# Performance work log

Hardware: AMD Instinct MI355X
Metric: run time of the kernel (lower is better)

The kernel has to match this reference:

```python
import jax, jax.numpy as jnp
import numpy as np

N_NODES = 100000
DEG = 16          # regular-graph degree so degrees[start] > 0 for all nodes
STEPS = 32
D_FEAT = 16
MAXI32 = 2147483647


def setup_inputs() -> dict:
    key = jax.random.key(0)
    k1, k2, k3 = jax.random.split(key, 3)
    x = jax.random.normal(k1, (N_NODES, D_FEAT), dtype=jnp.float32)
    # CSR-style flat adjacency list: node v's neighbors are
    # adj_nodes[adj_offset[v] : adj_offset[v] + degrees[v]]
    adj_nodes = jax.random.randint(k2, (N_NODES * DEG,), 0, N_NODES, dtype=jnp.int32)
    adj_offset = (jnp.arange(N_NODES, dtype=jnp.int32) * DEG)
    degrees = jnp.full((N_NODES,), DEG, dtype=jnp.int32)
    # cache of random integers, one per (step, walk), as in the torch code
    choices = jax.random.randint(k3, (STEPS, N_NODES), 0, MAXI32, dtype=jnp.int32)
    return {"x": x, "adj_nodes": adj_nodes, "adj_offset": adj_offset,
            "degrees": degrees, "choices": choices}


def reference(x, adj_nodes, adj_offset, degrees, choices):
    """Non-backtracking random walk (Walker.sample_walks with start_p=1.0,
    all nodes having degree > 0, so start = arange(n)).
    Returns walks [steps+1, w] and walk_edges [steps, w]."""
    n = degrees.shape[0]
    nb_degrees = jnp.maximum(degrees - 1, 1)  # reduced degree for non-backtrack rewrite
    start = jnp.arange(n, dtype=jnp.int32)

    def step(carry, ch):
        prev, cur = carry                      # [w] previous / current nodes
        deg = degrees[cur]
        edge_idx = ch % deg                    # unweighted modulo edge choice
        chosen = adj_offset[cur] + edge_idx
        new = adj_nodes[chosen]
        bt = new == prev                       # backtracking walks
        # conditional rewrite: pick a different outgoing edge
        alt = adj_offset[cur] + (edge_idx + 1 + ch % nb_degrees[cur]) % deg
        chosen = jnp.where(bt, alt, chosen)
        new = jnp.where(bt, adj_nodes[alt], new)
        return (cur, new), (new, chosen)

    # prev = -1 at step 0 => bt is all-False, matching the i > 0 guard
    prev0 = jnp.full_like(start, -1)
    _, (nodes, walk_edges) = jax.lax.scan(step, (prev0, start), choices)
    walks = jnp.concatenate([start[None, :], nodes], axis=0)  # [steps+1, w]
    return walks, walk_edges
```

## Files before the change

### kernel.cpp

```cpp
#include <hip/hip_runtime.h>
#include <hip/hip_bf16.h>


#define DEG 16

__global__ void check_kernel(const int* __restrict__ degrees,
                             const int* __restrict__ adj_offset,
                             int n, int* __restrict__ flag) {
    int v = blockIdx.x * blockDim.x + threadIdx.x;
    if (v < n) {
        if (degrees[v] != DEG || adj_offset[v] != v * DEG)
            atomicOr(flag, 1);
    }
}

template <int STEPS>
__global__ __launch_bounds__(256) void walker_fast(
    const int* __restrict__ adj_nodes,
    const int* __restrict__ adj_offset,
    const int* __restrict__ degrees,
    const int* __restrict__ choices,
    int* __restrict__ out, int n,
    const int* __restrict__ flag) {

    int w = blockIdx.x * blockDim.x + threadIdx.x;
    if (w >= n) return;

    int* walks      = out;
    int* walk_edges = out + (STEPS + 1) * n;
    walks[w] = w;

    if (*flag == 0) {
        int chs[STEPS];
#pragma unroll
        for (int i = 0; i < STEPS; ++i) chs[i] = choices[i * n + w];

        int prev = -1, cur = w;
#pragma unroll
        for (int i = 0; i < STEPS; ++i) {
            int ch   = chs[i];
            int e    = ch & (DEG - 1);
            int base = cur << 4;
            int chosen = base + e;
            int alt    = base + ((e + 1 + ch % (DEG - 1)) & (DEG - 1));

            int nw0 = adj_nodes[chosen];
            int nw1 = adj_nodes[alt];

            bool bt = (nw0 == prev);
            int nw  = bt ? nw1 : nw0;
            walks[(i + 1) * n + w] = nw;
            walk_edges[i * n + w]  = bt ? alt : chosen;
            prev = cur;
            cur  = nw;
        }
    } else {
        int prev = -1, cur = w;
        for (int i = 0; i < STEPS; ++i) {
            int ch  = choices[i * n + w];
            int deg = degrees[cur];
            int off = adj_offset[cur];
            int nb  = deg - 1 > 1 ? deg - 1 : 1;

            int e      = ch % deg;
            int chosen = off + e;
            int alt    = off + (e + 1 + ch % nb) % deg;

            int nw0 = adj_nodes[chosen];
            int nw1 = adj_nodes[alt];

            bool bt = (nw0 == prev);
            int nw  = bt ? nw1 : nw0;
            walks[(i + 1) * n + w] = nw;
            walk_edges[i * n + w]  = bt ? alt : chosen;
            prev = cur;
            cur  = nw;
        }
    }
}

__global__ __launch_bounds__(256) void walker_generic(
    const int* __restrict__ adj_nodes,
    const int* __restrict__ adj_offset,
    const int* __restrict__ degrees,
    const int* __restrict__ choices,
    int* __restrict__ out, int n, int steps) {

    int w = blockIdx.x * blockDim.x + threadIdx.x;
    if (w >= n) return;

    int* walks      = out;
    int* walk_edges = out + (steps + 1) * n;
    walks[w] = w;

    int prev = -1, cur = w;
    for (int i = 0; i < steps; ++i) {
        int ch  = choices[i * n + w];
        int deg = degrees[cur];
        int off = adj_offset[cur];
        int nb  = deg - 1 > 1 ? deg - 1 : 1;

        int e      = ch % deg;
        int chosen = off + e;
        int alt    = off + (e + 1 + ch % nb) % deg;

        int nw0 = adj_nodes[chosen];
        int nw1 = adj_nodes[alt];

        bool bt = (nw0 == prev);
        int nw  = bt ? nw1 : nw0;
        walks[(i + 1) * n + w] = nw;
        walk_edges[i * n + w]  = bt ? alt : chosen;
        prev = cur;
        cur  = nw;
    }
}

extern "C" void kernel_launch(void* const* d_in, const int* in_sizes, int n_in,
                              void* d_out, int out_size, void* d_ws, size_t ws_size,
                              hipStream_t stream) {
    const int* adj_nodes  = (const int*)d_in[1];
    const int* adj_offset = (const int*)d_in[2];
    const int* degrees    = (const int*)d_in[3];
    const int* choices    = (const int*)d_in[4];
    int* out  = (int*)d_out;
    int* flag = (int*)d_ws;

    int n     = in_sizes[2];
    int steps = in_sizes[4] / n;

    int block = 256;
    int grid  = (n + block - 1) / block;

    if (steps == 32) {
        hipMemsetAsync(flag, 0, sizeof(int), stream);
        check_kernel<<<grid, block, 0, stream>>>(degrees, adj_offset, n, flag);
        walker_fast<32><<<grid, block, 0, stream>>>(adj_nodes, adj_offset,
                                                    degrees, choices, out, n, flag);
    } else {
        walker_generic<<<grid, block, 0, stream>>>(adj_nodes, adj_offset,
                                                   degrees, choices, out, n, steps);
    }
}
```

Baseline: 118.6 us.

## Pack adjacency into 16-bit low halves plus per-row high-bit mask for walker gathers

Adds a pre-pass that repacks adj_nodes into 16-bit low values plus a 16-bit mask holding bit 16 of each entry, and validates that all node ids fit in 17 bits. The walker then gathers from this half-size table, aiming to make the dependent random gathers more cache-resident. It also switches output stores and choice loads to nontemporal and drops the block size to 128. The cost is an extra pass over the full adjacency on every call and a third gather per step for the high-bit mask.

```diff
diff --git a/kernel.cpp b/kernel.cpp
--- a/kernel.cpp
+++ b/kernel.cpp
@@ -4,22 +4,44 @@
 
 #define DEG 16
 
-__global__ void check_kernel(const int* __restrict__ degrees,
-                             const int* __restrict__ adj_offset,
-                             int n, int* __restrict__ flag) {
+__global__ void pack_check_kernel(const int* __restrict__ adj_nodes,
+                                  const int* __restrict__ adj_offset,
+                                  const int* __restrict__ degrees,
+                                  int n,
+                                  unsigned short* __restrict__ lo,
+                                  unsigned short* __restrict__ hi,
+                                  int* __restrict__ flag) {
     int v = blockIdx.x * blockDim.x + threadIdx.x;
-    if (v < n) {
-        if (degrees[v] != DEG || adj_offset[v] != v * DEG)
-            atomicOr(flag, 1);
+    if (v >= n) return;
+
+    bool bad = (degrees[v] != DEG) || (adj_offset[v] != v * DEG);
+
+    const int* row = adj_nodes + (size_t)v * DEG;
+    union { unsigned short u16[DEG]; uint4 v4[2]; } p;
+    unsigned hbits = 0;
+#pragma unroll
+    for (int j = 0; j < DEG; ++j) {
+        unsigned u = (unsigned)row[j];
+        if (u >= 131072u) bad = true;
+        p.u16[j] = (unsigned short)(u & 0xffffu);
+        hbits |= ((u >> 16) & 1u) << j;
     }
+    uint4* dst = (uint4*)(lo + (size_t)v * DEG);
+    dst[0] = p.v4[0];
+    dst[1] = p.v4[1];
+    hi[v] = (unsigned short)hbits;
+
+    if (bad) atomicOr(flag, 1);
 }
 
 template <int STEPS>
-__global__ __launch_bounds__(256) void walker_fast(
+__global__ __launch_bounds__(128) void walker_fast(
     const int* __restrict__ adj_nodes,
     const int* __restrict__ adj_offset,
     const int* __restrict__ degrees,
     const int* __restrict__ choices,
+    const unsigned short* __restrict__ lo,
+    const unsigned short* __restrict__ hi,
     int* __restrict__ out, int n,
     const int* __restrict__ flag) {
 
@@ -28,29 +50,33 @@
 
     int* walks      = out;
     int* walk_edges = out + (STEPS + 1) * n;
-    walks[w] = w;
+    __builtin_nontemporal_store(w, &walks[w]);
 
     if (*flag == 0) {
         int chs[STEPS];
 #pragma unroll
-        for (int i = 0; i < STEPS; ++i) chs[i] = choices[i * n + w];
+        for (int i = 0; i < STEPS; ++i)
+            chs[i] = __builtin_nontemporal_load(&choices[i * n + w]);
 
         int prev = -1, cur = w;
 #pragma unroll
         for (int i = 0; i < STEPS; ++i) {
-            int ch   = chs[i];
-            int e    = ch & (DEG - 1);
+            int ch  = chs[i];
+            int e   = ch & (DEG - 1);
+            int ae  = (e + 1 + ch % (DEG - 1)) & (DEG - 1);
             int base = cur << 4;
-            int chosen = base + e;
-            int alt    = base + ((e + 1 + ch % (DEG - 1)) & (DEG - 1));
 
-            int nw0 = adj_nodes[chosen];
-            int nw1 = adj_nodes[alt];
+            unsigned l0 = lo[base + e];
+            unsigned l1 = lo[base + ae];
+            unsigned hb = hi[cur];
+
+            int nw0 = (int)(l0 | (((hb >> e)  & 1u) << 16));
+            int nw1 = (int)(l1 | (((hb >> ae) & 1u) << 16));
 
             bool bt = (nw0 == prev);
             int nw  = bt ? nw1 : nw0;
-            walks[(i + 1) * n + w] = nw;
-            walk_edges[i * n + w]  = bt ? alt : chosen;
+            __builtin_nontemporal_store(nw, &walks[(i + 1) * n + w]);
+            __builtin_nontemporal_store(base + (bt ? ae : e), &walk_edges[i * n + w]);
             prev = cur;
             cur  = nw;
         }
@@ -123,21 +149,30 @@
     const int* adj_offset = (const int*)d_in[2];
     const int* degrees    = (const int*)d_in[3];
     const int* choices    = (const int*)d_in[4];
-    int* out  = (int*)d_out;
-    int* flag = (int*)d_ws;
+    int* out = (int*)d_out;
 
     int n     = in_sizes[2];
     int steps = in_sizes[4] / n;
 
-    int block = 256;
-    int grid  = (n + block - 1) / block;
+    size_t lo_off = 64;
+    size_t lo_bytes = (size_t)n * DEG * sizeof(unsigned short);
+    size_t hi_off = lo_off + ((lo_bytes + 63) & ~(size_t)63);
+    size_t need = hi_off + (size_t)n * sizeof(unsigned short);
 
-    if (steps == 32) {
+    if (steps == 32 && ws_size >= need) {
+        int* flag = (int*)d_ws;
+        unsigned short* lo = (unsigned short*)((char*)d_ws + lo_off);
+        unsigned short* hi = (unsigned short*)((char*)d_ws + hi_off);
+
         hipMemsetAsync(flag, 0, sizeof(int), stream);
-        check_kernel<<<grid, block, 0, stream>>>(degrees, adj_offset, n, flag);
-        walker_fast<32><<<grid, block, 0, stream>>>(adj_nodes, adj_offset,
-                                                    degrees, choices, out, n, flag);
+        int pb = 256, pg = (n + pb - 1) / pb;
+        pack_check_kernel<<<pg, pb, 0, stream>>>(adj_nodes, adj_offset, degrees,
+                                                 n, lo, hi, flag);
+        int wb = 128, wg = (n + wb - 1) / wb;
+        walker_fast<32><<<wg, wb, 0, stream>>>(adj_nodes, adj_offset, degrees,
+                                               choices, lo, hi, out, n, flag);
     } else {
+        int block = 256, grid = (n + block - 1) / block;
         walker_generic<<<grid, block, 0, stream>>>(adj_nodes, adj_offset,
                                                    degrees, choices, out, n, steps);
     }
```

Result: no change. 120.5 us (+1.6%).

## Pack adjacency into 17-bit compressed rows and walk two paths per thread

Applied to the files above, without the earlier changes.

A prepass kernel repacks each node's 16 neighbor IDs into 16-bit low halves plus a bitmask of high bits (36 bytes per row), while still checking the regular-graph assumption. The walker reads from this compact table, so each random row lookup touches about one cache line and the whole table is more likely to stay cache-resident. Each thread now advances two independent walks to overlap their dependent loads, and the kernel uses 64-thread blocks and nontemporal loads and stores. In exchange it pays for an extra full pass over adjacency each call, and nodes with IDs of 131072 or more, or workspace that is too small, fall back to slower paths.

```diff
diff --git a/kernel.cpp b/kernel.cpp
--- a/kernel.cpp
+++ b/kernel.cpp
@@ -4,77 +4,135 @@
 
 #define DEG 16
 
-__global__ void check_kernel(const int* __restrict__ degrees,
-                             const int* __restrict__ adj_offset,
-                             int n, int* __restrict__ flag) {
+__global__ void pack_check_kernel(const int* __restrict__ adj_nodes,
+                                  const int* __restrict__ adj_offset,
+                                  const int* __restrict__ degrees,
+                                  int n,
+                                  unsigned int* __restrict__ pk32,
+                                  int* __restrict__ flag) {
     int v = blockIdx.x * blockDim.x + threadIdx.x;
-    if (v < n) {
-        if (degrees[v] != DEG || adj_offset[v] != v * DEG)
-            atomicOr(flag, 1);
-    }
+    if (v >= n) return;
+
+    bool bad = (degrees[v] != DEG) || (adj_offset[v] != v * DEG);
+
+    const int* row = adj_nodes + (size_t)v * DEG;
+    unsigned w[8];
+    unsigned hbits = 0;
+#pragma unroll
+    for (int j = 0; j < 8; ++j) {
+        unsigned u0 = (unsigned)row[2 * j];
+        unsigned u1 = (unsigned)row[2 * j + 1];
+        if (u0 >= 131072u || u1 >= 131072u) bad = true;
+        w[j] = (u0 & 0xffffu) | ((u1 & 0xffffu) << 16);
+        hbits |= ((u0 >> 16) & 1u) << (2 * j);
+        hbits |= ((u1 >> 16) & 1u) << (2 * j + 1);
+    }
+    unsigned int* dst = pk32 + (size_t)v * 9;
+#pragma unroll
+    for (int j = 0; j < 8; ++j) dst[j] = w[j];
+    dst[8] = hbits;
+
+    if (bad) atomicOr(flag, 1);
 }
 
 template <int STEPS>
-__global__ __launch_bounds__(256) void walker_fast(
+__global__ __launch_bounds__(64) void walker_fast2(
+    const unsigned short* __restrict__ pk,
+    const int* __restrict__ choices,
+    int* __restrict__ out, int n, int h,
+    const int* __restrict__ flag,
     const int* __restrict__ adj_nodes,
     const int* __restrict__ adj_offset,
-    const int* __restrict__ degrees,
-    const int* __restrict__ choices,
-    int* __restrict__ out, int n,
-    const int* __restrict__ flag) {
-
-    int w = blockIdx.x * blockDim.x + threadIdx.x;
-    if (w >= n) return;
+    const int* __restrict__ degrees) {
+
+    int t = blockIdx.x * blockDim.x + threadIdx.x;
+    if (t >= h) return;
 
     int* walks      = out;
     int* walk_edges = out + (STEPS + 1) * n;
-    walks[w] = w;
+
+    int w0 = t;
+    int w1 = t + h;
+    bool has1 = (w1 < n);
+    int w1s = has1 ? w1 : w0;
+
+    __builtin_nontemporal_store(w0, &walks[w0]);
+    if (has1) __builtin_nontemporal_store(w1, &walks[w1]);
 
     if (*flag == 0) {
-        int chs[STEPS];
-#pragma unroll
-        for (int i = 0; i < STEPS; ++i) chs[i] = choices[i * n + w];
-
-        int prev = -1, cur = w;
+        int c0[STEPS], c1[STEPS];
 #pragma unroll
         for (int i = 0; i < STEPS; ++i) {
-            int ch   = chs[i];
-            int e    = ch & (DEG - 1);
-            int base = cur << 4;
-            int chosen = base + e;
-            int alt    = base + ((e + 1 + ch % (DEG - 1)) & (DEG - 1));
-
-            int nw0 = adj_nodes[chosen];
-            int nw1 = adj_nodes[alt];
-
-            bool bt = (nw0 == prev);
-            int nw  = bt ? nw1 : nw0;
-            walks[(i + 1) * n + w] = nw;
-            walk_edges[i * n + w]  = bt ? alt : chosen;
-            prev = cur;
-            cur  = nw;
+            c0[i] = __builtin_nontemporal_load(&choices[i * n + w0]);
+            c1[i] = __builtin_nontemporal_load(&choices[i * n + w1s]);
+        }
+
+        int prev0 = -1, cur0 = w0;
+        int prev1 = -1, cur1 = w1s;
+#pragma unroll
+        for (int i = 0; i < STEPS; ++i) {
+            int ch0 = c0[i], ch1 = c1[i];
+            int e0 = ch0 & (DEG - 1);
+            int e1 = ch1 & (DEG - 1);
+            int a0 = (e0 + 1 + ch0 % (DEG - 1)) & (DEG - 1);
+            int a1 = (e1 + 1 + ch1 % (DEG - 1)) & (DEG - 1);
+
+            const unsigned short* r0 = pk + (unsigned)cur0 * 18u;
+            const unsigned short* r1 = pk + (unsigned)cur1 * 18u;
+
+            unsigned l00 = r0[e0];
+            unsigned l01 = r0[a0];
+            unsigned hb0 = r0[16];
+            unsigned l10 = r1[e1];
+            unsigned l11 = r1[a1];
+            unsigned hb1 = r1[16];
+
+            int n00 = (int)(l00 | (((hb0 >> e0) & 1u) << 16));
+            int n01 = (int)(l01 | (((hb0 >> a0) & 1u) << 16));
+            int n10 = (int)(l10 | (((hb1 >> e1) & 1u) << 16));
+            int n11 = (int)(l11 | (((hb1 >> a1) & 1u) << 16));
+
+            bool bt0 = (n00 == prev0);
+            bool bt1 = (n10 == prev1);
+            int nw0 = bt0 ? n01 : n00;
+            int nw1 = bt1 ? n11 : n10;
+            int ce0 = (cur0 << 4) + (bt0 ? a0 : e0);
+            int ce1 = (cur1 << 4) + (bt1 ? a1 : e1);
+
+            __builtin_nontemporal_store(nw0, &walks[(i + 1) * n + w0]);
+            __builtin_nontemporal_store(ce0, &walk_edges[i * n + w0]);
+            if (has1) {
+                __builtin_nontemporal_store(nw1, &walks[(i + 1) * n + w1]);
+                __builtin_nontemporal_store(ce1, &walk_edges[i * n + w1]);
+            }
+            prev0 = cur0; cur0 = nw0;
+            prev1 = cur1; cur1 = nw1;
         }
     } else {
-        int prev = -1, cur = w;
-        for (int i = 0; i < STEPS; ++i) {
-            int ch  = choices[i * n + w];
-            int deg = degrees[cur];
-            int off = adj_offset[cur];
-            int nb  = deg - 1 > 1 ? deg - 1 : 1;
-
-            int e      = ch % deg;
-            int chosen = off + e;
-            int alt    = off + (e + 1 + ch % nb) % deg;
-
-            int nw0 = adj_nodes[chosen];
-            int nw1 = adj_nodes[alt];
-
-            bool bt = (nw0 == prev);
-            int nw  = bt ? nw1 : nw0;
-            walks[(i + 1) * n + w] = nw;
-            walk_edges[i * n + w]  = bt ? alt : chosen;
-            prev = cur;
-            cur  = nw;
+        for (int k = 0; k < 2; ++k) {
+            int w = (k == 0) ? w0 : w1;
+            if (w >= n) break;
+            int prev = -1, cur = w;
+            for (int i = 0; i < STEPS; ++i) {
+                int ch  = choices[i * n + w];
+                int deg = degrees[cur];
+                int off = adj_offset[cur];
+                int nb  = deg - 1 > 1 ? deg - 1 : 1;
+
+                int e      = ch % deg;
+                int chosen = off + e;
+                int alt    = off + (e + 1 + ch % nb) % deg;
+
+                int nv0 = adj_nodes[chosen];
+                int nv1 = adj_nodes[alt];
+
+                bool bt = (nv0 == prev);
+                int nw  = bt ? nv1 : nv0;
+                walks[(i + 1) * n + w] = nw;
+                walk_edges[i * n + w]  = bt ? alt : chosen;
+                prev = cur;
+                cur  = nw;
+            }
         }
     }
 }
@@ -104,11 +162,11 @@
         int chosen = off + e;
         int alt    = off + (e + 1 + ch % nb) % deg;
 
-        int nw0 = adj_nodes[chosen];
-        int nw1 = adj_nodes[alt];
-
-        bool bt = (nw0 == prev);
-        int nw  = bt ? nw1 : nw0;
+        int nv0 = adj_nodes[chosen];
+        int nv1 = adj_nodes[alt];
+
+        bool bt = (nv0 == prev);
+        int nw  = bt ? nv1 : nv0;
         walks[(i + 1) * n + w] = nw;
         walk_edges[i * n + w]  = bt ? alt : chosen;
         prev = cur;
@@ -123,21 +181,29 @@
     const int* adj_offset = (const int*)d_in[2];
     const int* degrees    = (const int*)d_in[3];
     const int* choices    = (const int*)d_in[4];
-    int* out  = (int*)d_out;
-    int* flag = (int*)d_ws;
+    int* out = (int*)d_out;
 
     int n     = in_sizes[2];
     int steps = in_sizes[4] / n;
 
-    int block = 256;
-    int grid  = (n + block - 1) / block;
-
-    if (steps == 32) {
+    size_t pk_off = 64;
+    size_t need   = pk_off + (size_t)n * 36;
+
+    if (steps == 32 && ws_size >= need) {
+        int* flag = (int*)d_ws;
+        unsigned int* pk32  = (unsigned int*)((char*)d_ws + pk_off);
+        unsigned short* pk  = (unsigned short*)pk32;
+
         hipMemsetAsync(flag, 0, sizeof(int), stream);
-        check_kernel<<<grid, block, 0, stream>>>(degrees, adj_offset, n, flag);
-        walker_fast<32><<<grid, block, 0, stream>>>(adj_nodes, adj_offset,
-                                                    degrees, choices, out, n, flag);
+        int pb = 256, pg = (n + pb - 1) / pb;
+        pack_check_kernel<<<pg, pb, 0, stream>>>(adj_nodes, adj_offset, degrees,
+                                                 n, pk32, flag);
+        int h  = (n + 1) / 2;
+        int wb = 64, wg = (h + wb - 1) / wb;
+        walker_fast2<32><<<wg, wb, 0, stream>>>(pk, choices, out, n, h, flag,
+                                                adj_nodes, adj_offset, degrees);
     } else {
+        int block = 256, grid = (n + block - 1) / block;
         walker_generic<<<grid, block, 0, stream>>>(adj_nodes, adj_offset,
                                                    degrees, choices, out, n, steps);
     }
```

Result: faster. 108.0 us (-8.9%).
